# Optimization experiments

Hardware: AMD Instinct MI355X
Metric: run time of the kernel (lower is better)

Reference implementation:

```python
import jax, jax.numpy as jnp
import numpy as np

N_HEAD = 8
T_THRESHOLD = 0.001


def setup_inputs() -> dict:
    key = jax.random.key(0)
    ks = jax.random.split(key, 5)
    B, N, NL, R = 4, 1024, 4, 256
    C = NL * R
    x = jax.random.normal(ks[0], (B, N, NL, R), dtype=jnp.float32)
    Wc = jax.random.normal(ks[1], (R, 3 * R), dtype=jnp.float32) * (1.0 / np.sqrt(R))
    bc = jnp.zeros((3 * R,), dtype=jnp.float32)
    Wp = jax.random.normal(ks[2], (C, C), dtype=jnp.float32) * (1.0 / np.sqrt(C))
    bp = jnp.zeros((C,), dtype=jnp.float32)
    return {"x": x, "Wc": Wc, "bc": bc, "Wp": Wp, "bp": bp}


def reference(x, Wc, bc, Wp, bp):
    B, N, NL, R = x.shape
    H = N_HEAD
    D = R // H  # head dim
    # shared per-level qkv projection: (B, N, NL, 3R)
    qkv = x @ Wc + bc
    q, k, v = jnp.split(qkv, 3, axis=-1)
    # split heads: (B, N, NL, H, D)
    q = q.reshape(B, N, NL, H, D)
    k = k.reshape(B, N, NL, H, D)
    v = v.reshape(B, N, NL, H, D)
    scale = 1.0 / np.sqrt(D).astype(np.float32)
    # per-level attention scores: (B, NL, H, N, N)
    att = jnp.einsum('bnlhd,bmlhd->blhnm', q, k) * scale
    att = jax.nn.softmax(att, axis=-1)
    # custom post-softmax thresholding (ReLU(softmax - T)); dropout is identity at eval
    att = jax.nn.relu(att - T_THRESHOLD)
    # multiply attentions across levels: low parent attention dooms the child
    comb = jnp.prod(att, axis=1)  # (B, H, N, N)
    # apply combined attention to each level's values: (B, N, NL, H, D)
    y = jnp.einsum('bhnm,bmlhd->bnlhd', comb, v)
    y = y.reshape(B, N, NL * H * D)  # (B, N, C)
    y = y @ Wp + bp  # c_proj; resid dropout identity at eval
    return y.reshape(B, N, NL, R)
```

## Files before the change

kernel.cpp:

```cpp
#include <hip/hip_runtime.h>

#define TTHR 0.001f
#define QSCALE 0.17677669529663687f
#define CAP 16
#define YSCALE 8388608.0f
#define YINV   1.1920928955078125e-07f

typedef _Float16 half4v __attribute__((ext_vector_type(4)));
typedef _Float16 half8v __attribute__((ext_vector_type(8)));
typedef float f32x4 __attribute__((ext_vector_type(4)));

__device__ __forceinline__ int xcd_bid() {
  return (blockIdx.x & 7) * ((int)gridDim.x >> 3) + ((int)blockIdx.x >> 3);
}

__device__ __forceinline__ void stage_tile_s(const _Float16* __restrict__ gsrc,
                                             int rowstride, _Float16* lds, int tid)
{
  const int lane = tid & 63;
  const int w4 = (tid >> 6) << 2;
#pragma unroll
  for (int r = 0; r < 4; ++r) {
    const int p = (w4 + r) * 64 + lane;
    const int row = p >> 3, xg = p & 7;
    __builtin_amdgcn_global_load_lds(
        (const __attribute__((address_space(1))) void*)(gsrc + row * rowstride + ((xg ^ (row & 7)) << 3)),
        (__attribute__((address_space(3))) void*)(lds + (w4 + r) * 512),
        16, 0, 0);
  }
}

__device__ __forceinline__ void stage_tile64(const _Float16* __restrict__ gsrc,
                                             int rowstride, _Float16* lds, int tid)
{
  const int lane = tid & 63;
  const int w2 = (tid >> 6) << 1;
#pragma unroll
  for (int r = 0; r < 2; ++r) {
    const int p = (w2 + r) * 64 + lane;
    const int row = p >> 3, xg = p & 7;
    __builtin_amdgcn_global_load_lds(
        (const __attribute__((address_space(1))) void*)(gsrc + row * rowstride + ((xg ^ (row & 7)) << 3)),
        (__attribute__((address_space(3))) void*)(lds + (w2 + r) * 512),
        16, 0, 0);
  }
}

__device__ __forceinline__ void stage_q64_512(const _Float16* __restrict__ gsrc,
                                              _Float16* lds, int tid)
{
  const int lane = tid & 63, w = tid >> 6;
  const int p = (w << 6) + lane;
  const int row = p >> 3, xg = p & 7;
  __builtin_amdgcn_global_load_lds(
      (const __attribute__((address_space(1))) void*)(gsrc + row * 64 + ((xg ^ (row & 7)) << 3)),
      (__attribute__((address_space(3))) void*)(lds + (w << 9)),
      16, 0, 0);
}

__device__ __forceinline__ void stage_k128_512(const _Float16* __restrict__ gsrc,
                                               _Float16* lds, int tid)
{
  const int lane = tid & 63, w = tid >> 6;
#pragma unroll
  for (int r = 0; r < 2; ++r) {
    const int p = ((w << 1) + r) * 64 + lane;
    const int row = p >> 3, xg = p & 7;
    __builtin_amdgcn_global_load_lds(
        (const __attribute__((address_space(1))) void*)(gsrc + row * 64 + ((xg ^ (row & 7)) << 3)),
        (__attribute__((address_space(3))) void*)(lds + ((w << 1) + r) * 512),
        16, 0, 0);
  }
}

__global__ __launch_bounds__(256) void k_split_rm(
    const float* __restrict__ in, _Float16* __restrict__ oh,
    _Float16* __restrict__ ol, int n4)
{
  const int i = blockIdx.x * 256 + threadIdx.x;
  if (i >= n4) return;
  float4 v = ((const float4*)in)[i];
  half4v h = {(_Float16)v.x, (_Float16)v.y, (_Float16)v.z, (_Float16)v.w};
  half4v l = {(_Float16)(v.x - (float)h[0]), (_Float16)(v.y - (float)h[1]),
              (_Float16)(v.z - (float)h[2]), (_Float16)(v.w - (float)h[3])};
  ((half4v*)oh)[i] = h;
  ((half4v*)ol)[i] = l;
}

__global__ __launch_bounds__(256) void k_split_tr(
    const float* __restrict__ in, _Float16* __restrict__ oh,
    _Float16* __restrict__ ol, int K, int N)
{
  __shared__ float t[32][33];
  const int nb = N >> 5;
  const int n0 = (blockIdx.x % nb) << 5, k0 = (blockIdx.x / nb) << 5;
  const int r = threadIdx.x >> 3, c4 = (threadIdx.x & 7) << 2;
  float4 v = *(const float4*)&in[(k0 + r) * N + n0 + c4];
  t[r][c4] = v.x; t[r][c4 + 1] = v.y; t[r][c4 + 2] = v.z; t[r][c4 + 3] = v.w;
  __syncthreads();
  float a0 = t[c4][r], a1 = t[c4 + 1][r], a2 = t[c4 + 2][r], a3 = t[c4 + 3][r];
  half4v h = {(_Float16)a0, (_Float16)a1, (_Float16)a2, (_Float16)a3};
  half4v l = {(_Float16)(a0 - (float)h[0]), (_Float16)(a1 - (float)h[1]),
              (_Float16)(a2 - (float)h[2]), (_Float16)(a3 - (float)h[3])};
  *(half4v*)&oh[(n0 + r) * K + k0 + c4] = h;
  *(half4v*)&ol[(n0 + r) * K + k0 + c4] = l;
}

template<int EPI>
__global__ __launch_bounds__(256) void k_gemm_split(
    const _Float16* __restrict__ Ah, const _Float16* __restrict__ Al,
    const _Float16* __restrict__ Bh, const _Float16* __restrict__ Bl,
    const float* __restrict__ bias, int K, int kclog, int nbn,
    float* __restrict__ out, _Float16* __restrict__ Qs,
    _Float16* __restrict__ Ks, float* __restrict__ Vp)
{
  __shared__ __align__(16) _Float16 Asm[2][8192];
  __shared__ __align__(16) _Float16 Bsm[2][4096];
  const int tid = threadIdx.x, lane = tid & 63, w = tid >> 6;
  const int wr = w >> 1, wc = w & 1;
  const int lrow = lane & 15, lk = lane >> 4;
  const int bid = xcd_bid();
  const int mt = bid / nbn, ct = bid % nbn;
  const int m0 = mt << 7, c0 = ct << 6;

  const int nch = 3 << kclog;
  const int kcm = (1 << kclog) - 1;
  stage_tile_s(Ah + (size_t)m0 * K, K, Asm[0], tid);
  stage_tile64(Bh + (size_t)c0 * K, K, Bsm[0], tid);
  __syncthreads();

  f32x4 acc[4][2] = {};
#pragma unroll 1
  for (int ch = 0; ch < nch; ++ch) {
    const int cur = ch & 1;
    if (ch + 1 < nch) {
      const int ch2 = ch + 1;
      const int phase = ch2 >> kclog, kc = ch2 & kcm;
      const _Float16* As = (phase == 2) ? Al : Ah;
      const _Float16* Bs = (phase == 1) ? Bl : Bh;
      stage_tile_s(As + (size_t)m0 * K + (kc << 6), K, Asm[cur ^ 1], tid);
      stage_tile64(Bs + (size_t)c0 * K + (kc << 6), K, Bsm[cur ^ 1], tid);
    }
#pragma unroll
    for (int ks = 0; ks < 2; ++ks) {
      half8v af[4], bf[2];
#pragma unroll
      for (int mi = 0; mi < 4; ++mi) {
        const int row = (wr << 6) + (mi << 4) + lrow;
        const int xg = ((ks << 2) + lk) ^ (row & 7);
        af[mi] = *(const half8v*)&Asm[cur][((row << 3) + xg) << 3];
      }
#pragma unroll
      for (int ni = 0; ni < 2; ++ni) {
        const int col = (wc << 5) + (ni << 4) + lrow;
        const int xg = ((ks << 2) + lk) ^ (col & 7);
        bf[ni] = *(const half8v*)&Bsm[cur][((col << 3) + xg) << 3];
      }
#pragma unroll
      for (int mi = 0; mi < 4; ++mi)
#pragma unroll
        for (int ni = 0; ni < 2; ++ni)
          acc[mi][ni] = __builtin_amdgcn_mfma_f32_16x16x32_f16(af[mi], bf[ni], acc[mi][ni], 0, 0, 0);
    }
    __syncthreads();
  }

#pragma unroll
  for (int ni = 0; ni < 2; ++ni) {
    const int c = c0 + (wc << 5) + (ni << 4) + lrow;
    const float bv = bias[c];
    if (EPI == 0) {
#pragma unroll
      for (int mi = 0; mi < 4; ++mi)
#pragma unroll
        for (int reg = 0; reg < 4; ++reg) {
          const int m = m0 + (wr << 6) + (mi << 4) + (lk << 2) + reg;
          out[m * 1024 + c] = acc[mi][ni][reg] * YINV + bv;
        }
    } else {
      const int part = c >> 8, cc = c & 255;
      const int h = cc >> 5, d = cc & 31;
#pragma unroll
      for (int mi = 0; mi < 4; ++mi)
#pragma unroll
        for (int reg = 0; reg < 4; ++reg) {
          const int m = m0 + (wr << 6) + (mi << 4) + (lk << 2) + reg;
          const int b = m >> 12, n = (m >> 2) & 1023, l = m & 3;
          const int panel = b * 32 + l * 8 + h;
          float v = acc[mi][ni][reg] + bv;
          if (part == 2) {
            Vp[(panel << 15) + n * 32 + d] = v;
          } else {
            _Float16* dst = part ? Ks : Qs;
            if (!part) v *= QSCALE;
            _Float16 hv = (_Float16)v;
            _Float16 lv = (_Float16)(v - (float)hv);
            dst[(panel << 16) + n * 64 + d] = hv;
            dst[(panel << 16) + n * 64 + 32 + d] = lv;
          }
        }
    }
  }
}

__global__ __launch_bounds__(256) void k_score_sum(
    const _Float16* __restrict__ Qs, const _Float16* __restrict__ Ks,
    float* __restrict__ Z)
{
  __shared__ __align__(16) _Float16 Qsm[8192];
  __shared__ __align__(16) _Float16 Ksm[2][8192];
  __shared__ float Zsh[128];
  const int tid = threadIdx.x, lane = tid & 63, w = tid >> 6;
  const int wr = w >> 1, wc = w & 1;
  const int lrow = lane & 15, lk = lane >> 4;
  const int bid = xcd_bid();
  const int rt = bid & 7, panel = bid >> 3;

  stage_tile_s(Qs + (panel << 16) + (rt << 13), 64, Qsm, tid);
  stage_tile_s(Ks + (panel << 16), 64, Ksm[0], tid);
  if (tid < 128) Zsh[tid] = 0.0f;
  __syncthreads();

  const int kstA[3] = {0, 0, 4}, kstB[3] = {0, 4, 0};
  half8v af[3][4];
#pragma unroll
  for (int ks = 0; ks < 3; ++ks)
#pragma unroll
    for (int mi = 0; mi < 4; ++mi) {
      const int row = (wr << 6) + (mi << 4) + lrow;
      const int xg = (kstA[ks] + lk) ^ (row & 7);
      af[ks][mi] = *(const half8v*)&Qsm[((row << 3) + xg) << 3];
    }

  float rsum[4][4] = {};
#pragma unroll 1
  for (int ct = 0; ct < 8; ++ct) {
    const int cur = ct & 1;
    if (ct < 7)
      stage_tile_s(Ks + (panel << 16) + ((ct + 1) << 13), 64, Ksm[cur ^ 1], tid);
    f32x4 acc[4][4] = {};
#pragma unroll
    for (int ks = 0; ks < 3; ++ks) {
      half8v bf[4];
#pragma unroll
      for (int ni = 0; ni < 4; ++ni) {
        const int col = (wc << 6) + (ni << 4) + lrow;
        const int xg = (kstB[ks] + lk) ^ (col & 7);
        bf[ni] = *(const half8v*)&Ksm[cur][((col << 3) + xg) << 3];
      }
#pragma unroll
      for (int mi = 0; mi < 4; ++mi)
#pragma unroll
        for (int ni = 0; ni < 4; ++ni)
          acc[mi][ni] = __builtin_amdgcn_mfma_f32_16x16x32_f16(af[ks][mi], bf[ni], acc[mi][ni], 0, 0, 0);
    }
#pragma unroll
    for (int mi = 0; mi < 4; ++mi)
#pragma unroll
      for (int reg = 0; reg < 4; ++reg)
#pragma unroll
        for (int ni = 0; ni < 4; ++ni)
          rsum[mi][reg] += __expf(acc[mi][ni][reg]);
    __syncthreads();
  }

#pragma unroll
  for (int mi = 0; mi < 4; ++mi)
#pragma unroll
    for (int reg = 0; reg < 4; ++reg) {
      float s = rsum[mi][reg];
      s += __shfl_xor(s, 1, 64);
      s += __shfl_xor(s, 2, 64);
      s += __shfl_xor(s, 4, 64);
      s += __shfl_xor(s, 8, 64);
      if (lrow == 0) atomicAdd(&Zsh[(wr << 6) + (mi << 4) + (lk << 2) + reg], s);
    }
  __syncthreads();
  if (tid < 128) Z[panel * 1024 + (rt << 7) + tid] = Zsh[tid];
}

__global__ __launch_bounds__(512) void k_comb2(
    const _Float16* __restrict__ Qs, const _Float16* __restrict__ Ks,
    const float* __restrict__ Z, int* __restrict__ ccnt,
    unsigned short* __restrict__ cidx, float* __restrict__ cval)
{
  __shared__ __align__(16) _Float16 Sm[2][12288];
  __shared__ float tzall[4][64];
  __shared__ float rz[64];
  __shared__ int lcnt[64];
  const int tid = threadIdx.x, lane = tid & 63, w = tid >> 6;
  const int wr = w >> 2, wc = w & 3;
  const int lrow = lane & 15, lk = lane >> 4;
  const int s = (blockIdx.x & 7) * 64 + ((int)blockIdx.x >> 3);
  const int bh = s >> 4, rt = s & 15;
  const int b = bh >> 3, h = bh & 7;
  const int pbase = b * 32 + h;

  stage_q64_512(Qs + (pbase << 16) + (rt << 12), Sm[0], tid);
  stage_k128_512(Ks + (pbase << 16), Sm[0] + 4096, tid);
  if (tid < 256) {
    const int l = tid >> 6, r = tid & 63;
    tzall[l][r] = TTHR * Z[(pbase + l * 8) * 1024 + (rt << 6) + r];
  }
  if (tid < 64) {
    const float* zp = Z + pbase * 1024 + (rt << 6) + tid;
    rz[tid] = 1.0f / ((zp[0] * zp[8192]) * (zp[16384] * zp[24576]));
  }
  __syncthreads();

  const int kstA[3] = {0, 0, 4}, kstB[3] = {0, 4, 0};
  float prod[2][2][4];

#pragma unroll 1
  for (int it = 0; it < 32; ++it) {
    const int l = it & 3, ct = it >> 2, cur = it & 1;
    if (it + 1 < 32) {
      const int l2 = (it + 1) & 3, ct2 = (it + 1) >> 2;
      _Float16* nb = Sm[cur ^ 1];
      stage_q64_512(Qs + ((pbase + l2 * 8) << 16) + (rt << 12), nb, tid);
      stage_k128_512(Ks + ((pbase + l2 * 8) << 16) + (ct2 << 13), nb + 4096, tid);
    }
    if (l == 0 && tid < 64) lcnt[tid] = 0;

    f32x4 acc[2][2] = {};
#pragma unroll
    for (int ks = 0; ks < 3; ++ks) {
      half8v af[2], bf[2];
#pragma unroll
      for (int mi = 0; mi < 2; ++mi) {
        const int row = (wr << 5) + (mi << 4) + lrow;
        const int xg = (kstA[ks] + lk) ^ (row & 7);
        af[mi] = *(const half8v*)&Sm[cur][((row << 3) + xg) << 3];
      }
#pragma unroll
      for (int ni = 0; ni < 2; ++ni) {
        const int col = (wc << 5) + (ni << 4) + lrow;
        const int xg = (kstB[ks] + lk) ^ (col & 7);
        bf[ni] = *(const half8v*)&Sm[cur][4096 + (((col << 3) + xg) << 3)];
      }
#pragma unroll
      for (int mi = 0; mi < 2; ++mi)
#pragma unroll
        for (int ni = 0; ni < 2; ++ni)
          acc[mi][ni] = __builtin_amdgcn_mfma_f32_16x16x32_f16(af[mi], bf[ni], acc[mi][ni], 0, 0, 0);
    }

#pragma unroll
    for (int mi = 0; mi < 2; ++mi)
#pragma unroll
      for (int reg = 0; reg < 4; ++reg) {
        const float tz = tzall[l][(wr << 5) + (mi << 4) + (lk << 2) + reg];
#pragma unroll
        for (int ni = 0; ni < 2; ++ni) {
          const float e = fmaxf(__expf(acc[mi][ni][reg]) - tz, 0.0f);
          prod[mi][ni][reg] = (l == 0) ? e : prod[mi][ni][reg] * e;
        }
      }

    if (l == 3) {
#pragma unroll
      for (int mi = 0; mi < 2; ++mi)
#pragma unroll
        for (int ni = 0; ni < 2; ++ni)
#pragma unroll
          for (int reg = 0; reg < 4; ++reg) {
            const int rloc = (wr << 5) + (mi << 4) + (lk << 2) + reg;
            const float v = prod[mi][ni][reg] * rz[rloc];
            if (v > 0.0f) {
              const int slot = atomicAdd(&lcnt[rloc], 1);
              if (slot < CAP) {
                const int rowc = (bh << 10) + (rt << 6) + rloc;
                const int mglob = (ct << 7) + (wc << 5) + (ni << 4) + lrow;
                cidx[(rowc * 8 + ct) * CAP + slot] = (unsigned short)mglob;
                cval[(rowc * 8 + ct) * CAP + slot] = v * YSCALE;
              }
            }
          }
      __syncthreads();
      if (tid < 64)
        ccnt[((bh << 10) + (rt << 6) + tid) * 8 + ct] = min(lcnt[tid], CAP);
    }
    __syncthreads();
  }
}

__global__ __launch_bounds__(512) void k_pv(
    const float* __restrict__ Vp, const int* __restrict__ ccnt,
    const unsigned short* __restrict__ cidx, const float* __restrict__ cval,
    _Float16* __restrict__ ysh, _Float16* __restrict__ ysl)
{
  const int rowc = blockIdx.x * 8 + (threadIdx.x >> 6);
  const int lane = threadIdx.x & 63;
  const int bh = rowc >> 10, n = rowc & 1023;
  const int b = bh >> 3, h = bh & 7;
  const int l0 = lane >> 5, d = lane & 31;
  const float* vA = Vp + ((b * 32 + l0 * 8 + h) << 15) + d;
  const float* vB = vA + (16 << 15);
  float y0 = 0.f, y1 = 0.f;
  for (int mcj = 0; mcj < 8; ++mcj) {
    const int cnt = ccnt[rowc * 8 + mcj];
    const int off = (rowc * 8 + mcj) * CAP;
    for (int i = 0; i < cnt; ++i) {
      const int m = cidx[off + i];
      const float w = cval[off + i];
      y0 = fmaf(w, vA[m * 32], y0);
      y1 = fmaf(w, vB[m * 32], y1);
    }
  }
  const int idx = ((b << 10) + n) * 1024 + l0 * 256 + h * 32 + d;
  _Float16 h0 = (_Float16)y0;
  ysh[idx] = h0;
  ysl[idx] = (_Float16)(y0 - (float)h0);
  _Float16 h1 = (_Float16)y1;
  ysh[idx + 512] = h1;
  ysl[idx + 512] = (_Float16)(y1 - (float)h1);
}

extern "C" void kernel_launch(void* const* d_in, const int* in_sizes, int n_in,
                              void* d_out, int out_size, void* d_ws, size_t ws_size,
                              hipStream_t stream)
{
  const float* x  = (const float*)d_in[0];
  const float* Wc = (const float*)d_in[1];
  const float* bc = (const float*)d_in[2];
  const float* Wp = (const float*)d_in[3];
  const float* bp = (const float*)d_in[4];
  float* out = (float*)d_out;
  (void)in_sizes; (void)n_in; (void)out_size;

  if (ws_size < 98828288ull) return;
  char* wsb = (char*)d_ws;
  float*          Vp   = (float*)wsb;
  _Float16*       Qs   = (_Float16*)(wsb + 16777216);
  _Float16*       Ks   = (_Float16*)(wsb + 33554432);
  float*          Z    = (float*)(wsb + 50331648);
  _Float16*       xh   = (_Float16*)(wsb + 50855936);
  _Float16*       xl   = (_Float16*)(wsb + 59244544);
  int*            ccnt = (int*)(wsb + 67633152);
  unsigned short* cidx = (unsigned short*)(wsb + 68681728);
  float*          cval = (float*)(wsb + 77070336);
  _Float16*       Wch  = (_Float16*)(wsb + 93847552);
  _Float16*       Wcl  = (_Float16*)(wsb + 94240768);
  _Float16*       Wph  = (_Float16*)(wsb + 94633984);
  _Float16*       Wpl  = (_Float16*)(wsb + 96731136);

  k_split_rm<<<dim3(4096), dim3(256), 0, stream>>>(x, xh, xl, 1048576);
  k_split_tr<<<dim3(192), dim3(256), 0, stream>>>(Wc, Wch, Wcl, 256, 768);
  k_split_tr<<<dim3(1024), dim3(256), 0, stream>>>(Wp, Wph, Wpl, 1024, 1024);
  k_gemm_split<1><<<dim3(1536), dim3(256), 0, stream>>>(
      xh, xl, Wch, Wcl, bc, 256, 2, 12, nullptr, Qs, Ks, Vp);
  k_score_sum<<<dim3(1024), dim3(256), 0, stream>>>(Qs, Ks, Z);
  k_comb2<<<dim3(512), dim3(512), 0, stream>>>(Qs, Ks, Z, ccnt, cidx, cval);
  k_pv<<<dim3(4096), dim3(512), 0, stream>>>(Vp, ccnt, cidx, cval, xh, xl);
  k_gemm_split<0><<<dim3(512), dim3(256), 0, stream>>>(
      xh, xl, Wph, Wpl, bp, 1024, 4, 16, out, nullptr, nullptr, nullptr);
}
```

Before: 225.2 us.

## Fuse score-sum into attention kernel, triple-buffer GEMM, use exp2

Merges the row-sum (softmax normaliser) kernel into the combined attention kernel. Each block keeps all four levels' Q tiles resident in LDS and runs two passes over K: the first computes the per-level Z sums and the second does thresholding and compaction. This removes the Z round-trip through global memory and one launch, but recomputes QK^T, which the separate score kernel already did. The split GEMM moves to a 3-stage LDS pipeline with manual vmcnt waits and a single barrier per chunk. Q is prescaled by log2(e) so exp2 can replace expf.

Result: no change. 228.5 us (+1.4%).

```diff
diff --git a/kernel.cpp b/kernel.cpp
--- a/kernel.cpp
+++ b/kernel.cpp
@@ -1,10 +1,16 @@
 #include <hip/hip_runtime.h>
 
 #define TTHR 0.001f
-#define QSCALE 0.17677669529663687f
+#define QSC2 0.25503486f
 #define CAP 16
 #define YSCALE 8388608.0f
 #define YINV   1.1920928955078125e-07f
+
+#if __has_builtin(__builtin_amdgcn_exp2f)
+#define EXP2(x) __builtin_amdgcn_exp2f(x)
+#else
+#define EXP2(x) __expf((x) * 0.6931471805599453f)
+#endif
 
 typedef _Float16 half4v __attribute__((ext_vector_type(4)));
 typedef _Float16 half8v __attribute__((ext_vector_type(8)));
@@ -114,8 +120,8 @@
     float* __restrict__ out, _Float16* __restrict__ Qs,
     _Float16* __restrict__ Ks, float* __restrict__ Vp)
 {
-  __shared__ __align__(16) _Float16 Asm[2][8192];
-  __shared__ __align__(16) _Float16 Bsm[2][4096];
+  __shared__ __align__(16) _Float16 Asm[3][8192];
+  __shared__ __align__(16) _Float16 Bsm[3][4096];
   const int tid = threadIdx.x, lane = tid & 63, w = tid >> 6;
   const int wr = w >> 1, wc = w & 1;
   const int lrow = lane & 15, lk = lane >> 4;
@@ -125,22 +131,31 @@
 
   const int nch = 3 << kclog;
   const int kcm = (1 << kclog) - 1;
-  stage_tile_s(Ah + (size_t)m0 * K, K, Asm[0], tid);
-  stage_tile64(Bh + (size_t)c0 * K, K, Bsm[0], tid);
-  __syncthreads();
+
+  auto abase = [&](int c2) -> const _Float16* {
+    const int phase = c2 >> kclog, kc = c2 & kcm;
+    const _Float16* A = (phase == 2) ? Al : Ah;
+    return A + (size_t)m0 * K + (kc << 6);
+  };
+  auto bbase = [&](int c2) -> const _Float16* {
+    const int phase = c2 >> kclog, kc = c2 & kcm;
+    const _Float16* B = (phase == 1) ? Bl : Bh;
+    return B + (size_t)c0 * K + (kc << 6);
+  };
+
+  stage_tile_s(abase(0), K, Asm[0], tid);
+  stage_tile64(bbase(0), K, Bsm[0], tid);
+  stage_tile_s(abase(1), K, Asm[1], tid);
+  stage_tile64(bbase(1), K, Bsm[1], tid);
 
   f32x4 acc[4][2] = {};
+  int cur = 0;
 #pragma unroll 1
   for (int ch = 0; ch < nch; ++ch) {
-    const int cur = ch & 1;
-    if (ch + 1 < nch) {
-      const int ch2 = ch + 1;
-      const int phase = ch2 >> kclog, kc = ch2 & kcm;
-      const _Float16* As = (phase == 2) ? Al : Ah;
-      const _Float16* Bs = (phase == 1) ? Bl : Bh;
-      stage_tile_s(As + (size_t)m0 * K + (kc << 6), K, Asm[cur ^ 1], tid);
-      stage_tile64(Bs + (size_t)c0 * K + (kc << 6), K, Bsm[cur ^ 1], tid);
-    }
+    if (ch + 1 < nch) { asm volatile("s_waitcnt vmcnt(6)" ::: "memory"); }
+    else              { asm volatile("s_waitcnt vmcnt(0)" ::: "memory"); }
+    __builtin_amdgcn_s_barrier();
+    __builtin_amdgcn_sched_barrier(0);
 #pragma unroll
     for (int ks = 0; ks < 2; ++ks) {
       half8v af[4], bf[2];
@@ -162,7 +177,12 @@
         for (int ni = 0; ni < 2; ++ni)
           acc[mi][ni] = __builtin_amdgcn_mfma_f32_16x16x32_f16(af[mi], bf[ni], acc[mi][ni], 0, 0, 0);
     }
-    __syncthreads();
+    if (ch + 2 < nch) {
+      int nb = cur + 2; if (nb >= 3) nb -= 3;
+      stage_tile_s(abase(ch + 2), K, Asm[nb], tid);
+      stage_tile64(bbase(ch + 2), K, Bsm[nb], tid);
+    }
+    ++cur; if (cur == 3) cur = 0;
   }
 
 #pragma unroll
@@ -192,7 +212,7 @@
             Vp[(panel << 15) + n * 32 + d] = v;
           } else {
             _Float16* dst = part ? Ks : Qs;
-            if (!part) v *= QSCALE;
+            if (!part) v *= QSC2;
             _Float16 hv = (_Float16)v;
             _Float16 lv = (_Float16)(v - (float)hv);
             dst[(panel << 16) + n * 64 + d] = hv;
@@ -203,89 +223,15 @@
   }
 }
 
-__global__ __launch_bounds__(256) void k_score_sum(
+__global__ __launch_bounds__(512) void k_att(
     const _Float16* __restrict__ Qs, const _Float16* __restrict__ Ks,
-    float* __restrict__ Z)
-{
-  __shared__ __align__(16) _Float16 Qsm[8192];
-  __shared__ __align__(16) _Float16 Ksm[2][8192];
-  __shared__ float Zsh[128];
-  const int tid = threadIdx.x, lane = tid & 63, w = tid >> 6;
-  const int wr = w >> 1, wc = w & 1;
-  const int lrow = lane & 15, lk = lane >> 4;
-  const int bid = xcd_bid();
-  const int rt = bid & 7, panel = bid >> 3;
-
-  stage_tile_s(Qs + (panel << 16) + (rt << 13), 64, Qsm, tid);
-  stage_tile_s(Ks + (panel << 16), 64, Ksm[0], tid);
-  if (tid < 128) Zsh[tid] = 0.0f;
-  __syncthreads();
-
-  const int kstA[3] = {0, 0, 4}, kstB[3] = {0, 4, 0};
-  half8v af[3][4];
-#pragma unroll
-  for (int ks = 0; ks < 3; ++ks)
-#pragma unroll
-    for (int mi = 0; mi < 4; ++mi) {
-      const int row = (wr << 6) + (mi << 4) + lrow;
-      const int xg = (kstA[ks] + lk) ^ (row & 7);
-      af[ks][mi] = *(const half8v*)&Qsm[((row << 3) + xg) << 3];
-    }
-
-  float rsum[4][4] = {};
-#pragma unroll 1
-  for (int ct = 0; ct < 8; ++ct) {
-    const int cur = ct & 1;
-    if (ct < 7)
-      stage_tile_s(Ks + (panel << 16) + ((ct + 1) << 13), 64, Ksm[cur ^ 1], tid);
-    f32x4 acc[4][4] = {};
-#pragma unroll
-    for (int ks = 0; ks < 3; ++ks) {
-      half8v bf[4];
-#pragma unroll
-      for (int ni = 0; ni < 4; ++ni) {
-        const int col = (wc << 6) + (ni << 4) + lrow;
-        const int xg = (kstB[ks] + lk) ^ (col & 7);
-        bf[ni] = *(const half8v*)&Ksm[cur][((col << 3) + xg) << 3];
-      }
-#pragma unroll
-      for (int mi = 0; mi < 4; ++mi)
-#pragma unroll
-        for (int ni = 0; ni < 4; ++ni)
-          acc[mi][ni] = __builtin_amdgcn_mfma_f32_16x16x32_f16(af[ks][mi], bf[ni], acc[mi][ni], 0, 0, 0);
-    }
-#pragma unroll
-    for (int mi = 0; mi < 4; ++mi)
-#pragma unroll
-      for (int reg = 0; reg < 4; ++reg)
-#pragma unroll
-        for (int ni = 0; ni < 4; ++ni)
-          rsum[mi][reg] += __expf(acc[mi][ni][reg]);
-    __syncthreads();
-  }
-
-#pragma unroll
-  for (int mi = 0; mi < 4; ++mi)
-#pragma unroll
-    for (int reg = 0; reg < 4; ++reg) {
-      float s = rsum[mi][reg];
-      s += __shfl_xor(s, 1, 64);
-      s += __shfl_xor(s, 2, 64);
-      s += __shfl_xor(s, 4, 64);
-      s += __shfl_xor(s, 8, 64);
-      if (lrow == 0) atomicAdd(&Zsh[(wr << 6) + (mi << 4) + (lk << 2) + reg], s);
-    }
-  __syncthreads();
-  if (tid < 128) Z[panel * 1024 + (rt << 7) + tid] = Zsh[tid];
-}
-
-__global__ __launch_bounds__(512) void k_comb2(
-    const _Float16* __restrict__ Qs, const _Float16* __restrict__ Ks,
-    const float* __restrict__ Z, int* __restrict__ ccnt,
-    unsigned short* __restrict__ cidx, float* __restrict__ cval)
-{
-  __shared__ __align__(16) _Float16 Sm[2][12288];
-  __shared__ float tzall[4][64];
+    int* __restrict__ ccnt, unsigned short* __restrict__ cidx,
+    float* __restrict__ cval)
+{
+  __shared__ __align__(16) _Float16 Qres[4][4096];
+  __shared__ __align__(16) _Float16 Kb[2][8192];
+  __shared__ float Zsh[4][64];
+  __shared__ float tzs[4][64];
   __shared__ float rz[64];
   __shared__ int lcnt[64];
   const int tid = threadIdx.x, lane = tid & 63, w = tid >> 6;
@@ -296,31 +242,30 @@
   const int b = bh >> 3, h = bh & 7;
   const int pbase = b * 32 + h;
 
-  stage_q64_512(Qs + (pbase << 16) + (rt << 12), Sm[0], tid);
-  stage_k128_512(Ks + (pbase << 16), Sm[0] + 4096, tid);
-  if (tid < 256) {
-    const int l = tid >> 6, r = tid & 63;
-    tzall[l][r] = TTHR * Z[(pbase + l * 8) * 1024 + (rt << 6) + r];
-  }
-  if (tid < 64) {
-    const float* zp = Z + pbase * 1024 + (rt << 6) + tid;
-    rz[tid] = 1.0f / ((zp[0] * zp[8192]) * (zp[16384] * zp[24576]));
-  }
+#pragma unroll
+  for (int l = 0; l < 4; ++l)
+    stage_q64_512(Qs + ((pbase + l * 8) << 16) + (rt << 12), Qres[l], tid);
+  stage_k128_512(Ks + (pbase << 16), Kb[0], tid);
+  if (tid < 256) Zsh[tid >> 6][tid & 63] = 0.0f;
   __syncthreads();
 
   const int kstA[3] = {0, 0, 4}, kstB[3] = {0, 4, 0};
+  float rsum[2][4] = {};
   float prod[2][2][4];
 
 #pragma unroll 1
-  for (int it = 0; it < 32; ++it) {
-    const int l = it & 3, ct = it >> 2, cur = it & 1;
-    if (it + 1 < 32) {
-      const int l2 = (it + 1) & 3, ct2 = (it + 1) >> 2;
-      _Float16* nb = Sm[cur ^ 1];
-      stage_q64_512(Qs + ((pbase + l2 * 8) << 16) + (rt << 12), nb, tid);
-      stage_k128_512(Ks + ((pbase + l2 * 8) << 16) + (ct2 << 13), nb + 4096, tid);
-    }
-    if (l == 0 && tid < 64) lcnt[tid] = 0;
+  for (int it = 0; it < 64; ++it) {
+    const int cur = it & 1;
+    const int pass = it >> 5;
+    const int l  = pass ? ((it - 32) & 3) : (it >> 3);
+    const int ct = pass ? ((it - 32) >> 2) : (it & 7);
+    if (it < 63) {
+      const int t2 = it + 1;
+      const int l2  = (t2 < 32) ? (t2 >> 3) : ((t2 - 32) & 3);
+      const int ct2 = (t2 < 32) ? (t2 & 7) : ((t2 - 32) >> 2);
+      stage_k128_512(Ks + ((pbase + l2 * 8) << 16) + (ct2 << 13), Kb[cur ^ 1], tid);
+    }
+    if (pass && l == 0 && tid < 64) lcnt[tid] = 0;
 
     f32x4 acc[2][2] = {};
 #pragma unroll
@@ -330,13 +275,13 @@
       for (int mi = 0; mi < 2; ++mi) {
         const int row = (wr << 5) + (mi << 4) + lrow;
         const int xg = (kstA[ks] + lk) ^ (row & 7);
-        af[mi] = *(const half8v*)&Sm[cur][((row << 3) + xg) << 3];
+        af[mi] = *(const half8v*)&Qres[l][((row << 3) + xg) << 3];
       }
 #pragma unroll
       for (int ni = 0; ni < 2; ++ni) {
         const int col = (wc << 5) + (ni << 4) + lrow;
         const int xg = (kstB[ks] + lk) ^ (col & 7);
-        bf[ni] = *(const half8v*)&Sm[cur][4096 + (((col << 3) + xg) << 3)];
+        bf[ni] = *(const half8v*)&Kb[cur][((col << 3) + xg) << 3];
       }
 #pragma unroll
       for (int mi = 0; mi < 2; ++mi)
@@ -345,42 +290,72 @@
           acc[mi][ni] = __builtin_amdgcn_mfma_f32_16x16x32_f16(af[mi], bf[ni], acc[mi][ni], 0, 0, 0);
     }
 
-#pragma unroll
-    for (int mi = 0; mi < 2; ++mi)
-#pragma unroll
-      for (int reg = 0; reg < 4; ++reg) {
-        const float tz = tzall[l][(wr << 5) + (mi << 4) + (lk << 2) + reg];
-#pragma unroll
-        for (int ni = 0; ni < 2; ++ni) {
-          const float e = fmaxf(__expf(acc[mi][ni][reg]) - tz, 0.0f);
-          prod[mi][ni][reg] = (l == 0) ? e : prod[mi][ni][reg] * e;
+    if (!pass) {
+#pragma unroll
+      for (int mi = 0; mi < 2; ++mi)
+#pragma unroll
+        for (int reg = 0; reg < 4; ++reg)
+#pragma unroll
+          for (int ni = 0; ni < 2; ++ni)
+            rsum[mi][reg] += EXP2(acc[mi][ni][reg]);
+      if ((it & 7) == 7) {
+#pragma unroll
+        for (int mi = 0; mi < 2; ++mi)
+#pragma unroll
+          for (int reg = 0; reg < 4; ++reg) {
+            float v = rsum[mi][reg];
+            v += __shfl_xor(v, 1, 64);
+            v += __shfl_xor(v, 2, 64);
+            v += __shfl_xor(v, 4, 64);
+            v += __shfl_xor(v, 8, 64);
+            if (lrow == 0)
+              atomicAdd(&Zsh[l][(wr << 5) + (mi << 4) + (lk << 2) + reg], v);
+            rsum[mi][reg] = 0.0f;
+          }
+      }
+    } else {
+#pragma unroll
+      for (int mi = 0; mi < 2; ++mi)
+#pragma unroll
+        for (int reg = 0; reg < 4; ++reg) {
+          const float tzv = tzs[l][(wr << 5) + (mi << 4) + (lk << 2) + reg];
+#pragma unroll
+          for (int ni = 0; ni < 2; ++ni) {
+            const float e = fmaxf(EXP2(acc[mi][ni][reg]) - tzv, 0.0f);
+            prod[mi][ni][reg] = (l == 0) ? e : prod[mi][ni][reg] * e;
+          }
         }
-      }
-
-    if (l == 3) {
-#pragma unroll
-      for (int mi = 0; mi < 2; ++mi)
-#pragma unroll
-        for (int ni = 0; ni < 2; ++ni)
-#pragma unroll
-          for (int reg = 0; reg < 4; ++reg) {
-            const int rloc = (wr << 5) + (mi << 4) + (lk << 2) + reg;
-            const float v = prod[mi][ni][reg] * rz[rloc];
-            if (v > 0.0f) {
-              const int slot = atomicAdd(&lcnt[rloc], 1);
-              if (slot < CAP) {
-                const int rowc = (bh << 10) + (rt << 6) + rloc;
-                const int mglob = (ct << 7) + (wc << 5) + (ni << 4) + lrow;
-                cidx[(rowc * 8 + ct) * CAP + slot] = (unsigned short)mglob;
-                cval[(rowc * 8 + ct) * CAP + slot] = v * YSCALE;
+      if (l == 3) {
+#pragma unroll
+        for (int mi = 0; mi < 2; ++mi)
+#pragma unroll
+          for (int ni = 0; ni < 2; ++ni)
+#pragma unroll
+            for (int reg = 0; reg < 4; ++reg) {
+              const int rloc = (wr << 5) + (mi << 4) + (lk << 2) + reg;
+              const float v = prod[mi][ni][reg] * rz[rloc];
+              if (v > 0.0f) {
+                const int slot = atomicAdd(&lcnt[rloc], 1);
+                if (slot < CAP) {
+                  const int rowc = (bh << 10) + (rt << 6) + rloc;
+                  const int mglob = (ct << 7) + (wc << 5) + (ni << 4) + lrow;
+                  cidx[(rowc * 8 + ct) * CAP + slot] = (unsigned short)mglob;
+                  cval[(rowc * 8 + ct) * CAP + slot] = v * YSCALE;
+                }
               }
             }
-          }
+        __syncthreads();
+        if (tid < 64)
+          ccnt[((bh << 10) + (rt << 6) + tid) * 8 + ct] = min(lcnt[tid], CAP);
+      }
+    }
+    __syncthreads();
+    if (it == 31) {
+      if (tid < 256) tzs[tid >> 6][tid & 63] = TTHR * Zsh[tid >> 6][tid & 63];
+      if (tid < 64)
+        rz[tid] = 1.0f / ((Zsh[0][tid] * Zsh[1][tid]) * (Zsh[2][tid] * Zsh[3][tid]));
       __syncthreads();
-      if (tid < 64)
-        ccnt[((bh << 10) + (rt << 6) + tid) * 8 + ct] = min(lcnt[tid], CAP);
-    }
-    __syncthreads();
+    }
   }
 }
 
@@ -402,9 +377,9 @@
     const int off = (rowc * 8 + mcj) * CAP;
     for (int i = 0; i < cnt; ++i) {
       const int m = cidx[off + i];
-      const float w = cval[off + i];
-      y0 = fmaf(w, vA[m * 32], y0);
-      y1 = fmaf(w, vB[m * 32], y1);
+      const float wv = cval[off + i];
+      y0 = fmaf(wv, vA[m * 32], y0);
+      y1 = fmaf(wv, vB[m * 32], y1);
     }
   }
   const int idx = ((b << 10) + n) * 1024 + l0 * 256 + h * 32 + d;
@@ -433,7 +408,6 @@
   float*          Vp   = (float*)wsb;
   _Float16*       Qs   = (_Float16*)(wsb + 16777216);
   _Float16*       Ks   = (_Float16*)(wsb + 33554432);
-  float*          Z    = (float*)(wsb + 50331648);
   _Float16*       xh   = (_Float16*)(wsb + 50855936);
   _Float16*       xl   = (_Float16*)(wsb + 59244544);
   int*            ccnt = (int*)(wsb + 67633152);
@@ -449,8 +423,7 @@
   k_split_tr<<<dim3(1024), dim3(256), 0, stream>>>(Wp, Wph, Wpl, 1024, 1024);
   k_gemm_split<1><<<dim3(1536), dim3(256), 0, stream>>>(
       xh, xl, Wch, Wcl, bc, 256, 2, 12, nullptr, Qs, Ks, Vp);
-  k_score_sum<<<dim3(1024), dim3(256), 0, stream>>>(Qs, Ks, Z);
-  k_comb2<<<dim3(512), dim3(512), 0, stream>>>(Qs, Ks, Z, ccnt, cidx, cval);
+  k_att<<<dim3(512), dim3(512), 0, stream>>>(Qs, Ks, ccnt, cidx, cval);
   k_pv<<<dim3(4096), dim3(512), 0, stream>>>(Vp, ccnt, cidx, cval, xh, xl);
   k_gemm_split<0><<<dim3(512), dim3(256), 0, stream>>>(
       xh, xl, Wph, Wpl, bp, 1024, 4, 16, out, nullptr, nullptr, nullptr);
```
